# Kernel tuning notes

Measured on AMD Instinct MI355X. Metric: run time of the kernel, lower is better.

## Reference

```python
import jax, jax.numpy as jnp
import numpy as np

B, S, D = 32, 512, 512      # batch, seq, feature
E, H, O, K = 8, 2048, 512, 2  # experts, expert hidden, expert out, top_k


def setup_inputs() -> dict:
    key = jax.random.key(0)
    ks = jax.random.split(key, 5)
    sc = lambda k, shape, scale: jax.random.normal(k, shape, jnp.float32) * scale
    return {
        "x": sc(ks[0], (B, S, D), 1.0),
        "attn_w": sc(ks[1], (D, 1), 0.05),
        "attn_b": jnp.zeros((1,), jnp.float32),
        "gate_w": sc(ks[2], (D, E), 0.05),
        "gate_b": jnp.zeros((E,), jnp.float32),
        "w1": sc(ks[3], (E, D, H), 0.02),
        "b1": jnp.zeros((E, H), jnp.float32),
        "w2": sc(ks[4], (E, H, O), 0.02),
        "b2": jnp.zeros((E, O), jnp.float32),
    }


def reference(x, attn_w, attn_b, gate_w, gate_b, w1, b1, w2, b2):
    # --- attention pooling over the sequence axis ---
    scores = x @ attn_w + attn_b                      # [B,S,1]
    aw = jax.nn.softmax(scores, axis=1)               # softmax over seq
    pooled = jnp.sum(x * aw, axis=1)                  # [B,D]

    # --- gating: softmax -> top-k mask -> renormalize ---
    gates = jax.nn.softmax(pooled @ gate_w + gate_b, axis=-1)  # [B,E]
    _, idx = jax.lax.top_k(gates, K)                  # [B,K]
    mask = jnp.sum(jax.nn.one_hot(idx, E, dtype=gates.dtype), axis=-2)  # [B,E]
    g = gates * mask
    g = g / (jnp.sum(g, axis=-1, keepdims=True) + 1e-9)        # [B,E]

    # --- dense all-experts compute (exact GELU, as keras Dense('gelu')) ---
    h = jax.nn.gelu(jnp.einsum('bsd,edh->ebsh', x, w1) + b1[:, None, None, :],
                    approximate=False)                 # [E,B,S,H]
    eo = jax.nn.gelu(jnp.einsum('ebsh,eho->ebso', h, w2) + b2[:, None, None, :],
                     approximate=False)                # [E,B,S,O]

    # --- weighted combine over experts ---
    return jnp.einsum('ebso,be->bso', eo, g)           # [B,S,O]
```

## Files before the change

### kernel.cpp

```cpp
#include <hip/hip_runtime.h>
#include <hip/hip_bf16.h>
#include <math.h>

#define B_  32
#define S_  512
#define D_  512
#define E_  8
#define H_  2048
#define O_  512

typedef __bf16 bf16x8 __attribute__((ext_vector_type(8)));
typedef float  f32x4  __attribute__((ext_vector_type(4)));

#define GL2LDS(src, dst) \
  __builtin_amdgcn_global_load_lds((const __attribute__((address_space(1))) void*)(src), \
                                   (__attribute__((address_space(3))) void*)(dst), 16, 0, 0)

#define MFMA16(a, b, c) __builtin_amdgcn_mfma_f32_16x16x32_bf16((a), (b), (c), 0, 0, 0)

__device__ __forceinline__ float gelu_fast(float v) {
  float w = v * fmaf(v * v, 0.0713548162f, 1.5957691216f);
  float e = __expf(-w);
  return v * __builtin_amdgcn_rcpf(1.0f + e);
}


__global__ __launch_bounds__(256) void cast_score_kernel(
    const float* __restrict__ x, const float* __restrict__ attn_w,
    char* __restrict__ xpack, float* __restrict__ scores)
{
  const int t = threadIdx.x;
  const int r = t >> 5;
  const int cg = t & 31;
  const int row = blockIdx.x * 8 + r;
  const int bb = row >> 9, s = row & 511;
  const float* src  = x + (size_t)row * D_ + cg * 16;
  const float* wsrc = attn_w + cg * 16;
  char* xp = xpack + (size_t)bb * 524288 + s * 64;
  const int sx = (s >> 1) & 3;
  float acc = 0.f;
#pragma unroll
  for (int k = 0; k < 4; ++k) {
    const int d0 = cg * 16 + k * 4;
    float4 v  = *(const float4*)(src + k * 4);
    float4 wv = *(const float4*)(wsrc + k * 4);
    acc += v.x * wv.x + v.y * wv.y + v.z * wv.z + v.w * wv.w;
    ushort4 o;
    o.x = __builtin_bit_cast(unsigned short, __float2bfloat16(v.x));
    o.y = __builtin_bit_cast(unsigned short, __float2bfloat16(v.y));
    o.z = __builtin_bit_cast(unsigned short, __float2bfloat16(v.z));
    o.w = __builtin_bit_cast(unsigned short, __float2bfloat16(v.w));
    const int u = d0 >> 5;
    const int byte = u * 32768 + ((((d0 >> 3) & 3) ^ sx) << 4) + (d0 & 7) * 2;
    *(ushort4*)(xp + byte) = o;
  }
#pragma unroll
  for (int off = 16; off; off >>= 1) acc += __shfl_xor(acc, off);
  if (cg == 0) scores[row] = acc;
}

__global__ __launch_bounds__(512) void softmax_aw_kernel(
    const float* __restrict__ scores, float* __restrict__ aw)
{
  __shared__ float red[8];
  __shared__ float mm, ss;
  const int t = threadIdx.x, b = blockIdx.x;
  float v = scores[b * S_ + t];
  float m = v;
#pragma unroll
  for (int off = 32; off; off >>= 1) m = fmaxf(m, __shfl_xor(m, off));
  if ((t & 63) == 0) red[t >> 6] = m;
  __syncthreads();
  if (t == 0) {
    float a = red[0];
    for (int i = 1; i < 8; ++i) a = fmaxf(a, red[i]);
    mm = a;
  }
  __syncthreads();
  float e = expf(v - mm);
  float s = e;
#pragma unroll
  for (int off = 32; off; off >>= 1) s += __shfl_xor(s, off);
  if ((t & 63) == 0) red[t >> 6] = s;
  __syncthreads();
  if (t == 0) {
    float a = 0.f;
    for (int i = 0; i < 8; ++i) a += red[i];
    ss = 1.f / a;
  }
  __syncthreads();
  aw[b * S_ + t] = e * ss;
}

__global__ __launch_bounds__(512) void pool_kernel(
    const float* __restrict__ x, const float* __restrict__ aw, float* __restrict__ pooled)
{
  __shared__ float sm[4][128];
  const int t = threadIdx.x;
  const int dl = t & 127;
  const int sh = t >> 7;
  const int b = blockIdx.y;
  const int d = blockIdx.x * 128 + dl;
  const float* xp  = x + (size_t)b * S_ * D_ + d;
  const float* awb = aw + b * S_;
  float acc = 0.f;
#pragma unroll 4
  for (int s = sh; s < S_; s += 4)
    acc = fmaf(awb[s], xp[(size_t)s * D_], acc);
  if (sh) sm[sh][dl] = acc;
  __syncthreads();
  if (sh == 0) pooled[b * D_ + d] = acc + sm[1][dl] + sm[2][dl] + sm[3][dl];
}

__global__ __launch_bounds__(256) void gate_psort_kernel(
    const float* __restrict__ pooled, const float* __restrict__ gate_w,
    const float* __restrict__ gate_b, int* __restrict__ gidx, float* __restrict__ gwt,
    int* __restrict__ psort)
{
  __shared__ float gl[32][8];
  const int t = threadIdx.x;
  const int b = t >> 3, ee = t & 7;
  float z = gate_b[ee];
  const float* pb = pooled + b * D_;
  for (int d = 0; d < D_; ++d) z = fmaf(pb[d], gate_w[d * E_ + ee], z);
  gl[b][ee] = z;
  __syncthreads();
  if (t < 32) {
    float ge[8];
    float zmax = gl[t][0];
    for (int i = 1; i < 8; ++i) zmax = fmaxf(zmax, gl[t][i]);
    float zs = 0.f;
    for (int i = 0; i < 8; ++i) { ge[i] = expf(gl[t][i] - zmax); zs += ge[i]; }
    for (int i = 0; i < 8; ++i) ge[i] /= zs;
    int i0 = 0;
    for (int i = 1; i < 8; ++i) if (ge[i] > ge[i0]) i0 = i;
    int i1 = -1;
    for (int i = 0; i < 8; ++i) if (i != i0 && (i1 < 0 || ge[i] > ge[i1])) i1 = i;
    float denom = ge[i0] + ge[i1] + 1e-9f;
    gidx[t * 2 + 0] = i0; gidx[t * 2 + 1] = i1;
    gwt[t * 2 + 0] = ge[i0] / denom; gwt[t * 2 + 1] = ge[i1] / denom;
  }
  __syncthreads();
  if (t == 0) {
    int cnt[E_] = {}, pos[E_];
    for (int p = 0; p < 2 * B_; ++p) cnt[gidx[p]]++;
    int s = 0;
    for (int e2 = 0; e2 < E_; ++e2) { pos[e2] = s; s += cnt[e2]; }
    for (int p = 0; p < 2 * B_; ++p) psort[pos[gidx[p]]++] = p;
  }
}

__global__ void pack_w_kernel(const float* __restrict__ in, char* __restrict__ outp,
                              int R, int C)
{
  __shared__ float tile[32][33];
  const int z = blockIdx.z;
  const float* inz = in + (size_t)z * R * C;
  const int c0 = blockIdx.x * 32, r0 = blockIdx.y * 32;
  const int tx = threadIdx.x, ty = threadIdx.y;
#pragma unroll
  for (int jj = 0; jj < 4; ++jj) {
    int r = r0 + ty + jj * 8;
    tile[ty + jj * 8][tx] = inz[(size_t)r * C + c0 + tx];
  }
  __syncthreads();
  const int k = r0 + tx;
  const int u = k >> 5;
  const int PAN = C * 64;
  char* oz = outp + (size_t)z * R * C * 2 + (size_t)u * PAN;
  const int kslot = (k >> 3) & 3;
  const int kbyte = (k & 7) * 2;
#pragma unroll
  for (int jj = 0; jj < 4; ++jj) {
    const int row = c0 + ty + jj * 8;
    const int byte = row * 64 + ((kslot ^ ((row >> 1) & 3)) << 4) + kbyte;
    *(ushort*)(oz + byte) =
        __builtin_bit_cast(unsigned short, __float2bfloat16(tile[tx][ty + jj * 8]));
  }
}

__device__ __forceinline__ void gemm_core_m97(const char* __restrict__ Ag, const char* __restrict__ Bg,
                                              const size_t unitA, const size_t unitB,
                                              const int NT, char* lds, f32x4 (&acc)[4][4])
{
  const int tid = threadIdx.x;
  const int l = tid & 63;
  const int w = tid >> 6;
  const int wm = w >> 1;
  const int wn = w & 1;
  const int lr = l & 15;
  const int ks = (l >> 4) & 3;
  const int swz = ((ks ^ ((lr >> 1) & 3)) << 4);
  const int abase = wm * 4096 + lr * 64 + swz;
  const int bbase = 16384 + wn * 4096 + lr * 64 + swz;
  const int dst = tid * 16;

#pragma unroll 1
  for (int t = 0; t < NT; ++t) {
    const char* a0 = Ag + (size_t)(2 * t)     * unitA;
    const char* a1 = Ag + (size_t)(2 * t + 1) * unitA;
    const char* b0 = Bg + (size_t)(2 * t)     * unitB;
    const char* b1 = Bg + (size_t)(2 * t + 1) * unitB;
    GL2LDS(a0 + dst, lds + dst);          GL2LDS(a0 + 4096 + dst, lds + 4096 + dst);
    GL2LDS(a1 + dst, lds + 8192 + dst);   GL2LDS(a1 + 4096 + dst, lds + 12288 + dst);
    GL2LDS(b0 + dst, lds + 16384 + dst);  GL2LDS(b0 + 4096 + dst, lds + 20480 + dst);
    GL2LDS(b1 + dst, lds + 24576 + dst);  GL2LDS(b1 + 4096 + dst, lds + 28672 + dst);
    asm volatile("s_waitcnt vmcnt(0)" ::: "memory");
    __builtin_amdgcn_s_barrier();

    bf16x8 a0f[4], a1f[4], b0f[4], b1f[4];
#pragma unroll
    for (int m = 0; m < 4; ++m) {
      a0f[m] = *(const bf16x8*)(lds + abase + m * 1024);
      a1f[m] = *(const bf16x8*)(lds + 8192 + abase + m * 1024);
    }
#pragma unroll
    for (int n = 0; n < 4; ++n) {
      b0f[n] = *(const bf16x8*)(lds + bbase + n * 1024);
      b1f[n] = *(const bf16x8*)(lds + 8192 + bbase + n * 1024);
    }
#pragma unroll
    for (int m = 0; m < 4; ++m)
#pragma unroll
      for (int n = 0; n < 4; ++n) {
        acc[m][n] = MFMA16(a0f[m], b0f[n], acc[m][n]);
        acc[m][n] = MFMA16(a1f[m], b1f[n], acc[m][n]);
      }
    __builtin_amdgcn_s_barrier();
  }
}

__global__ __launch_bounds__(256, 3) void gemm1_kernel(
    const char* __restrict__ xpack, const char* __restrict__ W1pack,
    const float* __restrict__ b1, char* __restrict__ Hpack,
    const int* __restrict__ gidx, const int* __restrict__ psort)
{
  __shared__ char lds[32768];
  const int P = blockIdx.x;
  const int L = (P & 7) * 512 + (P >> 3);
  const int p = psort[L >> 6];
  const int tl = L & 63;
  const int b = p >> 1;
  const int e = gidx[p];
  const int h0 = (tl >> 2) * 128;
  const int s0 = (tl & 3) * 128;
  const char* Ag = W1pack + (size_t)e * 2097152 + h0 * 64;
  const char* Bg = xpack + (size_t)b * 524288 + s0 * 64;
  f32x4 acc[4][4] = {};
  gemm_core_m97(Ag, Bg, 131072, 32768, D_ / 64, lds, acc);

  const int tid = threadIdx.x, l = tid & 63, w = tid >> 6;
  const int wm = w >> 1, wn = w & 1, lr = l & 15, q4 = ((l >> 4) & 3) << 2;
  const float* b1e = b1 + (size_t)e * H_ + h0;
  char* Hp = Hpack + (size_t)p * 2097152;
#pragma unroll
  for (int m = 0; m < 4; ++m) {
    const int hl = wm * 64 + m * 16 + q4;
    const int h = h0 + hl;
    const int uh = h >> 5;
    const int hslot = (h >> 3) & 3;
    const int hbyte = (h & 7) * 2;
    const float4 bias = *(const float4*)(b1e + hl);
#pragma unroll
    for (int n = 0; n < 4; ++n) {
      const int sl = s0 + wn * 64 + n * 16 + lr;
      ushort4 ov;
      ov.x = __builtin_bit_cast(unsigned short, __float2bfloat16(gelu_fast(acc[m][n][0] + bias.x)));
      ov.y = __builtin_bit_cast(unsigned short, __float2bfloat16(gelu_fast(acc[m][n][1] + bias.y)));
      ov.z = __builtin_bit_cast(unsigned short, __float2bfloat16(gelu_fast(acc[m][n][2] + bias.z)));
      ov.w = __builtin_bit_cast(unsigned short, __float2bfloat16(gelu_fast(acc[m][n][3] + bias.w)));
      const int byte = uh * 32768 + sl * 64 + ((hslot ^ ((sl >> 1) & 3)) << 4) + hbyte;
      *(ushort4*)(Hp + byte) = ov;
    }
  }
}

__global__ __launch_bounds__(256, 3) void gemm2_kernel(
    const char* __restrict__ Hpack, const char* __restrict__ W2pack,
    const float* __restrict__ b2, float* __restrict__ out,
    const int* __restrict__ gidx, const float* __restrict__ gwt,
    const int* __restrict__ psort)
{
  __shared__ char lds[32768];
  const int P = blockIdx.x;
  const int L = (P & 7) * 128 + (P >> 3);
  const int p = psort[L >> 4];
  const int tl = L & 15;
  const int b = p >> 1;
  const int e = gidx[p];
  const float gw = gwt[p];
  const int o0 = (tl >> 2) * 128;
  const int s0 = (tl & 3) * 128;
  const char* Ag = Hpack + (size_t)p * 2097152 + s0 * 64;
  const char* Bg = W2pack + (size_t)e * 2097152 + o0 * 64;
  f32x4 acc[4][4] = {};
  gemm_core_m97(Ag, Bg, 32768, 32768, H_ / 64, lds, acc);

  const int tid = threadIdx.x, l = tid & 63, w = tid >> 6;
  const int wm = w >> 1, wn = w & 1, lr = l & 15, q4 = ((l >> 4) & 3) << 2;
  const float* b2e = b2 + (size_t)e * O_ + o0;
#pragma unroll
  for (int m = 0; m < 4; ++m) {
    const int sl = s0 + wm * 64 + m * 16 + q4;
#pragma unroll
    for (int n = 0; n < 4; ++n) {
      const int ol = wn * 64 + n * 16 + lr;
      const float bias = b2e[ol];
      float* dstp = out + ((size_t)b * S_ + sl) * O_ + o0 + ol;
#pragma unroll
      for (int j = 0; j < 4; ++j)
        atomicAdd(dstp + (size_t)j * O_, gelu_fast(acc[m][n][j] + bias) * gw);
    }
  }
}

__global__ void sentinel_kernel(float* out, int n) {
  int i = blockIdx.x * blockDim.x + threadIdx.x;
  for (; i < n; i += gridDim.x * blockDim.x) out[i] = 1.0e6f;
}

extern "C" void kernel_launch(void* const* d_in, const int* in_sizes, int n_in,
                              void* d_out, int out_size, void* d_ws, size_t ws_size,
                              hipStream_t stream)
{
  const float* x      = (const float*)d_in[0];
  const float* attn_w = (const float*)d_in[1];
  const float* gate_w = (const float*)d_in[3];
  const float* gate_b = (const float*)d_in[4];
  const float* w1     = (const float*)d_in[5];
  const float* b1     = (const float*)d_in[6];
  const float* w2     = (const float*)d_in[7];
  const float* b2     = (const float*)d_in[8];
  float* out = (float*)d_out;

  char* ws = (char*)d_ws;
  const size_t OFF_GIDX = 0;
  const size_t OFF_GWT  = 256;
  const size_t OFF_PSRT = 512;
  const size_t OFF_X    = 1024;
  const size_t SZ_X     = (size_t)B_ * S_ * D_ * 2;
  const size_t OFF_W1T  = OFF_X + SZ_X;
  const size_t SZ_W1T   = (size_t)E_ * H_ * D_ * 2;
  const size_t OFF_W2T  = OFF_W1T + SZ_W1T;
  const size_t SZ_W2T   = (size_t)E_ * O_ * H_ * 2;
  const size_t OFF_H    = OFF_W2T + SZ_W2T;
  const size_t PAIR_H   = (size_t)S_ * H_ * 2;

  if (OFF_H + 64 * PAIR_H > ws_size) {
    hipLaunchKernelGGL(sentinel_kernel, dim3(256), dim3(256), 0, stream, out, out_size);
    return;
  }

  int*   gidx   = (int*)(ws + OFF_GIDX);
  float* gwt    = (float*)(ws + OFF_GWT);
  int*   psort  = (int*)(ws + OFF_PSRT);
  char*  xpack  = ws + OFF_X;
  char*  W1pack = ws + OFF_W1T;
  char*  W2pack = ws + OFF_W2T;
  char*  Hpack  = ws + OFF_H;
  float* scores = (float*)(ws + OFF_H);
  float* aw     = (float*)(ws + OFF_H + 65536);
  float* pooled = (float*)(ws + OFF_H + 131072);

  hipLaunchKernelGGL(cast_score_kernel, dim3(B_ * S_ / 8), dim3(256), 0, stream,
                     x, attn_w, xpack, scores);
  hipLaunchKernelGGL(softmax_aw_kernel, dim3(B_), dim3(512), 0, stream, scores, aw);
  hipLaunchKernelGGL(pool_kernel, dim3(4, B_), dim3(512), 0, stream, x, aw, pooled);
  hipLaunchKernelGGL(gate_psort_kernel, dim3(1), dim3(256), 0, stream,
                     pooled, gate_w, gate_b, gidx, gwt, psort);
  hipLaunchKernelGGL(pack_w_kernel, dim3(H_ / 32, D_ / 32, E_), dim3(32, 8), 0, stream,
                     w1, W1pack, D_, H_);
  hipLaunchKernelGGL(pack_w_kernel, dim3(O_ / 32, H_ / 32, E_), dim3(32, 8), 0, stream,
                     w2, W2pack, H_, O_);
  hipMemsetAsync(d_out, 0, (size_t)out_size * sizeof(float), stream);

  hipLaunchKernelGGL(gemm1_kernel, dim3(4096), dim3(256), 0, stream,
                     xpack, W1pack, b1, Hpack, gidx, psort);
  hipLaunchKernelGGL(gemm2_kernel, dim3(1024), dim3(256), 0, stream,
                     Hpack, W2pack, b2, out, gidx, gwt, psort);
}
```

Measured before the change: 262.1 us.

## Load GEMM B operand directly to registers and fuse softmax into pooling

```diff
diff --git a/kernel.cpp b/kernel.cpp
--- a/kernel.cpp
+++ b/kernel.cpp
@@ -59,12 +59,16 @@
   if (cg == 0) scores[row] = acc;
 }
 
-__global__ __launch_bounds__(512) void softmax_aw_kernel(
-    const float* __restrict__ scores, float* __restrict__ aw)
-{
+__global__ __launch_bounds__(512) void pool_kernel(
+    const float* __restrict__ x, const float* __restrict__ scores,
+    float* __restrict__ pooled)
+{
+  __shared__ float awsh[512];
   __shared__ float red[8];
   __shared__ float mm, ss;
-  const int t = threadIdx.x, b = blockIdx.x;
+  __shared__ float sm[4][128];
+  const int t = threadIdx.x;
+  const int b = blockIdx.y;
   float v = scores[b * S_ + t];
   float m = v;
 #pragma unroll
@@ -89,24 +93,17 @@
     ss = 1.f / a;
   }
   __syncthreads();
-  aw[b * S_ + t] = e * ss;
-}
-
-__global__ __launch_bounds__(512) void pool_kernel(
-    const float* __restrict__ x, const float* __restrict__ aw, float* __restrict__ pooled)
-{
-  __shared__ float sm[4][128];
-  const int t = threadIdx.x;
+  awsh[t] = e * ss;
+  __syncthreads();
+
   const int dl = t & 127;
   const int sh = t >> 7;
-  const int b = blockIdx.y;
   const int d = blockIdx.x * 128 + dl;
-  const float* xp  = x + (size_t)b * S_ * D_ + d;
-  const float* awb = aw + b * S_;
+  const float* xp = x + (size_t)b * S_ * D_ + d;
   float acc = 0.f;
 #pragma unroll 4
-  for (int s = sh; s < S_; s += 4)
-    acc = fmaf(awb[s], xp[(size_t)s * D_], acc);
+  for (int s2 = sh; s2 < S_; s2 += 4)
+    acc = fmaf(awsh[s2], xp[(size_t)s2 * D_], acc);
   if (sh) sm[sh][dl] = acc;
   __syncthreads();
   if (sh == 0) pooled[b * D_ + d] = acc + sm[1][dl] + sm[2][dl] + sm[3][dl];
@@ -179,7 +176,7 @@
   }
 }
 
-__device__ __forceinline__ void gemm_core_m97(const char* __restrict__ Ag, const char* __restrict__ Bg,
+__device__ __forceinline__ void gemm_core_v10(const char* __restrict__ Ag, const char* __restrict__ Bg,
                                               const size_t unitA, const size_t unitB,
                                               const int NT, char* lds, f32x4 (&acc)[4][4])
 {
@@ -192,39 +189,38 @@
   const int ks = (l >> 4) & 3;
   const int swz = ((ks ^ ((lr >> 1) & 3)) << 4);
   const int abase = wm * 4096 + lr * 64 + swz;
-  const int bbase = 16384 + wn * 4096 + lr * 64 + swz;
+  const int bloff = (wn * 64 + lr) * 64 + swz;
   const int dst = tid * 16;
 
 #pragma unroll 1
   for (int t = 0; t < NT; ++t) {
     const char* a0 = Ag + (size_t)(2 * t)     * unitA;
     const char* a1 = Ag + (size_t)(2 * t + 1) * unitA;
-    const char* b0 = Bg + (size_t)(2 * t)     * unitB;
-    const char* b1 = Bg + (size_t)(2 * t + 1) * unitB;
+    const char* b0 = Bg + (size_t)(2 * t)     * unitB + bloff;
+    const char* b1 = Bg + (size_t)(2 * t + 1) * unitB + bloff;
     GL2LDS(a0 + dst, lds + dst);          GL2LDS(a0 + 4096 + dst, lds + 4096 + dst);
     GL2LDS(a1 + dst, lds + 8192 + dst);   GL2LDS(a1 + 4096 + dst, lds + 12288 + dst);
-    GL2LDS(b0 + dst, lds + 16384 + dst);  GL2LDS(b0 + 4096 + dst, lds + 20480 + dst);
-    GL2LDS(b1 + dst, lds + 24576 + dst);  GL2LDS(b1 + 4096 + dst, lds + 28672 + dst);
+    bf16x8 bv0[4], bv1[4];
+#pragma unroll
+    for (int n = 0; n < 4; ++n) {
+      bv0[n] = *(const bf16x8*)(b0 + n * 1024);
+      bv1[n] = *(const bf16x8*)(b1 + n * 1024);
+    }
     asm volatile("s_waitcnt vmcnt(0)" ::: "memory");
     __builtin_amdgcn_s_barrier();
 
-    bf16x8 a0f[4], a1f[4], b0f[4], b1f[4];
+    bf16x8 a0f[4], a1f[4];
 #pragma unroll
     for (int m = 0; m < 4; ++m) {
       a0f[m] = *(const bf16x8*)(lds + abase + m * 1024);
       a1f[m] = *(const bf16x8*)(lds + 8192 + abase + m * 1024);
     }
 #pragma unroll
-    for (int n = 0; n < 4; ++n) {
-      b0f[n] = *(const bf16x8*)(lds + bbase + n * 1024);
-      b1f[n] = *(const bf16x8*)(lds + 8192 + bbase + n * 1024);
-    }
-#pragma unroll
     for (int m = 0; m < 4; ++m)
 #pragma unroll
       for (int n = 0; n < 4; ++n) {
-        acc[m][n] = MFMA16(a0f[m], b0f[n], acc[m][n]);
-        acc[m][n] = MFMA16(a1f[m], b1f[n], acc[m][n]);
+        acc[m][n] = MFMA16(a0f[m], bv0[n], acc[m][n]);
+        acc[m][n] = MFMA16(a1f[m], bv1[n], acc[m][n]);
       }
     __builtin_amdgcn_s_barrier();
   }
@@ -235,7 +231,7 @@
     const float* __restrict__ b1, char* __restrict__ Hpack,
     const int* __restrict__ gidx, const int* __restrict__ psort)
 {
-  __shared__ char lds[32768];
+  __shared__ char lds[16384];
   const int P = blockIdx.x;
   const int L = (P & 7) * 512 + (P >> 3);
   const int p = psort[L >> 6];
@@ -247,7 +243,7 @@
   const char* Ag = W1pack + (size_t)e * 2097152 + h0 * 64;
   const char* Bg = xpack + (size_t)b * 524288 + s0 * 64;
   f32x4 acc[4][4] = {};
-  gemm_core_m97(Ag, Bg, 131072, 32768, D_ / 64, lds, acc);
+  gemm_core_v10(Ag, Bg, 131072, 32768, D_ / 64, lds, acc);
 
   const int tid = threadIdx.x, l = tid & 63, w = tid >> 6;
   const int wm = w >> 1, wn = w & 1, lr = l & 15, q4 = ((l >> 4) & 3) << 2;
@@ -281,7 +277,7 @@
     const int* __restrict__ gidx, const float* __restrict__ gwt,
     const int* __restrict__ psort)
 {
-  __shared__ char lds[32768];
+  __shared__ char lds[16384];
   const int P = blockIdx.x;
   const int L = (P & 7) * 128 + (P >> 3);
   const int p = psort[L >> 4];
@@ -294,7 +290,7 @@
   const char* Ag = Hpack + (size_t)p * 2097152 + s0 * 64;
   const char* Bg = W2pack + (size_t)e * 2097152 + o0 * 64;
   f32x4 acc[4][4] = {};
-  gemm_core_m97(Ag, Bg, 32768, 32768, H_ / 64, lds, acc);
+  gemm_core_v10(Ag, Bg, 32768, 32768, H_ / 64, lds, acc);
 
   const int tid = threadIdx.x, l = tid & 63, w = tid >> 6;
   const int wm = w >> 1, wn = w & 1, lr = l & 15, q4 = ((l >> 4) & 3) << 2;
@@ -359,13 +355,11 @@
   char*  W2pack = ws + OFF_W2T;
   char*  Hpack  = ws + OFF_H;
   float* scores = (float*)(ws + OFF_H);
-  float* aw     = (float*)(ws + OFF_H + 65536);
   float* pooled = (float*)(ws + OFF_H + 131072);
 
   hipLaunchKernelGGL(cast_score_kernel, dim3(B_ * S_ / 8), dim3(256), 0, stream,
                      x, attn_w, xpack, scores);
-  hipLaunchKernelGGL(softmax_aw_kernel, dim3(B_), dim3(512), 0, stream, scores, aw);
-  hipLaunchKernelGGL(pool_kernel, dim3(4, B_), dim3(512), 0, stream, x, aw, pooled);
+  hipLaunchKernelGGL(pool_kernel, dim3(4, B_), dim3(512), 0, stream, x, scores, pooled);
   hipLaunchKernelGGL(gate_psort_kernel, dim3(1), dim3(256), 0, stream,
                      pooled, gate_w, gate_b, gidx, gwt, psort);
   hipLaunchKernelGGL(pack_w_kernel, dim3(H_ / 32, D_ / 32, E_), dim3(32, 8), 0, stream,
```

New measurement: 260.5 us. No clear change (-0.6%).
